# Performance work log

Hardware: AMD Instinct MI355X
Metric: run time of the kernel (lower is better)

Reference implementation:

```python
import jax, jax.numpy as jnp
import numpy as np

NUM_CLASSES = 21
OVERLAP_THRESH = 0.5
POS_PRIOR_THRESH = 0.01
NEGPOS_RATIO = 3
ARM_VAR = (0.1, 0.2)
VAR = (0.1, 0.2)
B, P, NOBJ = 64, 16320, 32


def _iou(a, b):
    # a: [N,4] point-form, b: [P,4] point-form -> [N,P]
    lt = jnp.maximum(a[:, None, :2], b[None, :, :2])
    rb = jnp.minimum(a[:, None, 2:], b[None, :, 2:])
    wh = jnp.clip(rb - lt, 0.0)
    inter = wh[..., 0] * wh[..., 1]
    area_a = (a[:, 2] - a[:, 0]) * (a[:, 3] - a[:, 1])
    area_b = (b[:, 2] - b[:, 0]) * (b[:, 3] - b[:, 1])
    return inter / (area_a[:, None] + area_b[None, :] - inter)


def _decode_point(loc, priors, var):
    # loc: [P,4], priors: [P,4] center-form -> [P,4] point-form
    cxcy = priors[:, :2] + loc[:, :2] * var[0] * priors[:, 2:]
    wh = priors[:, 2:] * jnp.exp(loc[:, 2:] * var[1])
    return jnp.concatenate([cxcy - wh / 2, cxcy + wh / 2], axis=-1)


def _encode(matched, priors, var):
    # matched: [P,4] point-form gt, priors: [P,4] center-form -> [P,4]
    g_cxcy = ((matched[:, :2] + matched[:, 2:]) / 2 - priors[:, :2]) / (var[0] * priors[:, 2:])
    g_wh = jnp.log((matched[:, 2:] - matched[:, :2]) / priors[:, 2:]) / var[1]
    return jnp.concatenate([g_cxcy, g_wh], axis=-1)


def _match_one(truths, labels, dec_point, ref_center, reserve):
    # truths:[N,4] labels:[N] dec_point/ref_center:[P,4] reserve:[P] bool
    n_obj = truths.shape[0]
    ov = _iou(truths, dec_point)                       # [N,P]
    ovm = jnp.where(reserve[None, :], ov, -1.0)        # mask out filtered priors
    best_prior_idx = jnp.argmax(ovm, axis=1)           # [N]
    best_truth_overlap = jnp.max(ovm, axis=0)          # [P]
    best_truth_idx = jnp.argmax(ovm, axis=0)           # [P]
    best_truth_overlap = best_truth_overlap.at[best_prior_idx].set(2.0)
    best_truth_idx = best_truth_idx.at[best_prior_idx].set(jnp.arange(n_obj))
    matched = truths[best_truth_idx]                   # [P,4]
    conf = labels[best_truth_idx] + 1                  # [P]
    conf = jnp.where(best_truth_overlap < OVERLAP_THRESH, 0, conf)
    loc = _encode(matched, ref_center, VAR)
    conf = jnp.where(reserve, conf, -1)                # ignored priors
    loc = jnp.where(reserve[:, None], loc, 0.0)
    return loc, conf


def setup_inputs() -> dict:
    key = jax.random.key(0)
    ks = jax.random.split(key, 8)
    arm_loc = 0.1 * jax.random.normal(ks[0], (B, P, 4), dtype=jnp.float32)
    arm_conf = jax.random.normal(ks[1], (B, P, 2), dtype=jnp.float32)
    odm_loc = jax.random.normal(ks[2], (B, P, 4), dtype=jnp.float32)
    odm_conf = jax.random.normal(ks[3], (B, P, NUM_CLASSES), dtype=jnp.float32)
    # center-form anchors: valid cx,cy,w,h
    cxcy = jax.random.uniform(ks[4], (P, 2), minval=0.02, maxval=0.98)
    wh = jax.random.uniform(ks[5], (P, 2), minval=0.05, maxval=0.4)
    priors = jnp.concatenate([cxcy, wh], axis=-1).astype(jnp.float32)
    # valid point-form ground-truth boxes
    tc = jax.random.uniform(ks[6], (B, NOBJ, 2), minval=0.2, maxval=0.8)
    tw = jax.random.uniform(ks[7], (B, NOBJ, 2), minval=0.05, maxval=0.3)
    truths = jnp.concatenate([tc - tw / 2, tc + tw / 2], axis=-1).astype(jnp.float32)
    labels = jax.random.randint(jax.random.fold_in(key, 9), (B, NOBJ), 0, 20)
    return {"arm_loc": arm_loc, "arm_conf": arm_conf, "odm_loc": odm_loc,
            "odm_conf": odm_conf, "priors": priors, "truths": truths,
            "labels": labels}


def reference(arm_loc, arm_conf, odm_loc, odm_conf, priors, truths, labels):
    # ARM branch and targets are constants w.r.t. gradients (torch uses .data)
    arm_loc = jax.lax.stop_gradient(arm_loc)
    arm_conf = jax.lax.stop_gradient(arm_conf)
    truths = jax.lax.stop_gradient(truths)
    priors = jax.lax.stop_gradient(priors)

    arm_pos_prob = jax.nn.softmax(arm_conf, axis=-1)[..., 1]       # [B,P]
    reserve = arm_pos_prob > POS_PRIOR_THRESH                      # [B,P]
    dec_point = jax.vmap(lambda l: _decode_point(l, priors, ARM_VAR))(arm_loc)  # [B,P,4]
    ref_center = jnp.concatenate([(dec_point[..., :2] + dec_point[..., 2:]) / 2,
                                  dec_point[..., 2:] - dec_point[..., :2]], axis=-1)
    loc_t, conf_t = jax.vmap(_match_one)(truths, labels, dec_point, ref_center, reserve)
    loc_t = jax.lax.stop_gradient(loc_t)
    conf_t = jax.lax.stop_gradient(conf_t)

    pos = conf_t > 0                                               # [B,P]
    ignore = conf_t == -1
    conf_t0 = jnp.where(ignore, 0, conf_t)

    # localization: smooth L1 over positives (sum)
    d = jnp.abs(odm_loc - loc_t)
    sl1 = jnp.where(d < 1.0, 0.5 * d * d, d - 0.5)
    loss_l = jnp.sum(sl1 * pos[..., None].astype(sl1.dtype))

    # per-prior CE: logsumexp - target logit
    lse = jax.nn.logsumexp(odm_conf, axis=-1)                      # [B,P]
    tgt = jnp.take_along_axis(odm_conf, conf_t0[..., None], axis=-1)[..., 0]
    ce = lse - tgt                                                 # [B,P]

    # hard-negative mining: rank negatives by CE (double argsort)
    mine = jnp.where(pos | ignore, 0.0, ce)
    order = jnp.argsort(-mine, axis=1)
    rank = jnp.argsort(order, axis=1)
    num_pos = jnp.sum(pos, axis=1, keepdims=True)                  # [B,1]
    num_neg = jnp.minimum(NEGPOS_RATIO * num_pos, P - 1)
    neg = rank < num_neg

    loss_c = jnp.sum(jnp.where(pos | neg, ce, 0.0))
    total_num = jnp.sum(num_pos).astype(jnp.float32)
    return (loss_l / total_num, loss_c / total_num)
```

## Files before the change

### kernel.cpp

```cpp
#include <hip/hip_runtime.h>

#define B 64
#define P 16320
#define NOBJ 32
#define NC 21

constexpr int T1 = 512;
constexpr int G1 = 4;
constexpr int C1 = T1 * G1;
constexpr int NP1 = (P + C1 - 1) / C1;
constexpr int BLK2 = 256;
constexpr int PBLK2 = (P + BLK2 - 1) / BLK2;
constexpr int TSEL = 1024;
__device__ constexpr float LN99 = 4.59511985013459f;

__global__ void k_init(unsigned long long* bp_packed, int* num_pos, float* ll_b, float* lc_b) {
    int t = threadIdx.x;
    for (int i = t; i < B * NOBJ; i += 256) bp_packed[i] = 0x407FFFFFFFFFFFFFULL;
    if (t < B) { num_pos[t] = 0; ll_b[t] = 0.f; lc_b[t] = 0.f; }
}

__global__ __launch_bounds__(T1) void k_phase1(
    const float* __restrict__ arm_loc, const float* __restrict__ arm_conf,
    const float* __restrict__ priors, const float* __restrict__ truths,
    int* __restrict__ bt_pack, unsigned long long* __restrict__ bp_packed)
{
    int b = blockIdx.y;
    int base = blockIdx.x * C1;
    int tid = threadIdx.x;
    __shared__ float4 tr4[NOBJ];
    __shared__ float tarea[NOBJ];
    __shared__ unsigned long long blk_best[NOBJ];
    if (tid < NOBJ) {
        float4 t = ((const float4*)truths)[b * NOBJ + tid];
        tr4[tid] = t;
        tarea[tid] = (t.z - t.x) * (t.w - t.y);
        blk_best[tid] = 0ULL;
    }
    __syncthreads();

    float x1[G1], y1[G1], x2[G1], y2[G1], areaP[G1];
    bool resv[G1], act[G1];
    float bestv[G1]; int bestj[G1];
    #pragma unroll
    for (int g = 0; g < G1; g++) {
        int p = base + g * T1 + tid;
        act[g] = p < P;
        resv[g] = false;
        x1[g] = y1[g] = x2[g] = y2[g] = 0.f; areaP[g] = 0.f;
        bestv[g] = -1.f; bestj[g] = 0;
        if (act[g]) {
            size_t bpi = (size_t)b * P + p;
            float2 cc = ((const float2*)arm_conf)[bpi];
            resv[g] = (cc.x - cc.y) < LN99;
            float4 l = ((const float4*)arm_loc)[bpi];
            float4 pr = ((const float4*)priors)[p];
            float dcx = pr.x + l.x * 0.1f * pr.z;
            float dcy = pr.y + l.y * 0.1f * pr.w;
            float dw = pr.z * __expf(l.z * 0.2f);
            float dh = pr.w * __expf(l.w * 0.2f);
            x1[g] = dcx - dw * 0.5f; y1[g] = dcy - dh * 0.5f;
            x2[g] = dcx + dw * 0.5f; y2[g] = dcy + dh * 0.5f;
            areaP[g] = (x2[g] - x1[g]) * (y2[g] - y1[g]);
        }
    }

    float val[NOBJ];
    unsigned gsel[2] = {0u, 0u};
    #pragma unroll
    for (int j = 0; j < NOBJ; j++) val[j] = -1.f;

    #pragma unroll
    for (int j = 0; j < NOBJ; j++) {
        float4 t = tr4[j];
        float ta = tarea[j];
        #pragma unroll
        for (int g = 0; g < G1; g++) {
            float iw = fmaxf(fminf(x2[g], t.z) - fmaxf(x1[g], t.x), 0.f);
            float ih = fmaxf(fminf(y2[g], t.w) - fmaxf(y1[g], t.y), 0.f);
            float inter = iw * ih;
            float iou = inter * __builtin_amdgcn_rcpf(ta + areaP[g] - inter);
            if (resv[g] && iou > bestv[g]) { bestv[g] = iou; bestj[g] = j; }
            if (resv[g] && iou > val[j]) {
                val[j] = iou;
                gsel[j >> 4] = (gsel[j >> 4] & ~(3u << (2 * (j & 15))))
                             | ((unsigned)g << (2 * (j & 15)));
            }
        }
    }

    #pragma unroll
    for (int g = 0; g < G1; g++) {
        if (act[g]) {
            int p = base + g * T1 + tid;
            int ge = (resv[g] && !(bestv[g] < 0.5f)) ? 1 : 0;
            bt_pack[(size_t)b * P + p] = (bestj[g] << 1) | ge;
        }
    }

    #pragma unroll
    for (int j = 0; j < NOBJ; j++) {
        unsigned g = (gsel[j >> 4] >> (2 * (j & 15))) & 3u;
        unsigned p = (unsigned)(base + (int)g * T1 + tid);
        unsigned long long pk = (val[j] >= 0.f)
            ? (((unsigned long long)(__float_as_uint(val[j]) | 0x80000000u) << 32)
               | (unsigned)~p)
            : 0ULL;
        #pragma unroll
        for (int off = 32; off; off >>= 1) {
            unsigned long long o = __shfl_xor(pk, off, 64);
            pk = o > pk ? o : pk;
        }
        if ((tid & 63) == 0 && pk) atomicMax(&blk_best[j], pk);
    }
    __syncthreads();
    if (tid < NOBJ && blk_best[tid]) atomicMax(&bp_packed[b * NOBJ + tid], blk_best[tid]);
}

__global__ __launch_bounds__(BLK2) void k_phase2(
    const float* __restrict__ arm_loc, const float* __restrict__ arm_conf,
    const float* __restrict__ odm_loc, const float* __restrict__ odm_conf,
    const float* __restrict__ priors, const float* __restrict__ truths,
    const int* __restrict__ labels, const int* __restrict__ bt_pack,
    const unsigned long long* __restrict__ bp_packed,
    float* __restrict__ mine, int* __restrict__ num_pos,
    float* __restrict__ ll_b, float* __restrict__ lc_b)
{
    int b = blockIdx.y;
    int p = blockIdx.x * BLK2 + threadIdx.x;
    __shared__ unsigned s_pi[NOBJ];
    __shared__ int s_lab[NOBJ];
    if (threadIdx.x < NOBJ) {
        s_pi[threadIdx.x] = ~(unsigned)(bp_packed[b * NOBJ + threadIdx.x] & 0xFFFFFFFFULL);
        s_lab[threadIdx.x] = labels[b * NOBJ + threadIdx.x];
    }
    __syncthreads();

    float ll = 0.f, lc = 0.f; int np = 0;
    if (p < P) {
        size_t bpi = (size_t)b * P + p;
        float2 cc = ((const float2*)arm_conf)[bpi];
        bool reserve = (cc.x - cc.y) < LN99;

        int pk = bt_pack[bpi];
        int bi = pk >> 1;
        int ge = pk & 1;
        #pragma unroll
        for (int j = 0; j < NOBJ; j++)
            if (s_pi[j] == (unsigned)p) { ge = 1; bi = j; }

        int conf = !reserve ? -1 : (ge ? s_lab[bi] + 1 : 0);

        const float* oc = odm_conf + bpi * NC;
        float vals[NC];
        #pragma unroll
        for (int k = 0; k < NC; k++) vals[k] = oc[k];
        float m = vals[0];
        #pragma unroll
        for (int k = 1; k < NC; k++) m = fmaxf(m, vals[k]);
        float s = 0.f;
        #pragma unroll
        for (int k = 0; k < NC; k++) s += __expf(vals[k] - m);
        int t0 = conf > 0 ? conf : 0;
        float ce = m + __logf(s) - oc[t0];

        bool pos = conf > 0;
        mine[bpi] = (pos || conf == -1) ? 0.f : ce;

        if (pos) {
            np = 1; lc = ce;
            float4 l = ((const float4*)arm_loc)[bpi];
            float4 pr = ((const float4*)priors)[p];
            float dcx = pr.x + l.x * 0.1f * pr.z;
            float dcy = pr.y + l.y * 0.1f * pr.w;
            float dw = pr.z * __expf(l.z * 0.2f);
            float dh = pr.w * __expf(l.w * 0.2f);
            float rx1 = dcx - dw * 0.5f, ry1 = dcy - dh * 0.5f;
            float rx2 = dcx + dw * 0.5f, ry2 = dcy + dh * 0.5f;
            float rcx = (rx1 + rx2) * 0.5f, rcy = (ry1 + ry2) * 0.5f;
            float rw = rx2 - rx1, rh = ry2 - ry1;
            float4 tb = ((const float4*)truths)[b * NOBJ + bi];
            float g0 = ((tb.x + tb.z) * 0.5f - rcx) * __builtin_amdgcn_rcpf(0.1f * rw);
            float g1 = ((tb.y + tb.w) * 0.5f - rcy) * __builtin_amdgcn_rcpf(0.1f * rh);
            float g2 = __logf((tb.z - tb.x) * __builtin_amdgcn_rcpf(rw)) * 5.0f;
            float g3 = __logf((tb.w - tb.y) * __builtin_amdgcn_rcpf(rh)) * 5.0f;
            float4 ol = ((const float4*)odm_loc)[bpi];
            float gt[4] = {g0, g1, g2, g3};
            float od[4] = {ol.x, ol.y, ol.z, ol.w};
            #pragma unroll
            for (int k = 0; k < 4; k++) {
                float d = fabsf(od[k] - gt[k]);
                ll += (d < 1.f) ? 0.5f * d * d : d - 0.5f;
            }
        }
    }

    #pragma unroll
    for (int off = 32; off; off >>= 1) {
        ll += __shfl_xor(ll, off, 64);
        lc += __shfl_xor(lc, off, 64);
        np += __shfl_xor(np, off, 64);
    }
    __shared__ float sll[BLK2 / 64], slc[BLK2 / 64];
    __shared__ int snp[BLK2 / 64];
    int wid = threadIdx.x >> 6, lane = threadIdx.x & 63;
    if (lane == 0) { sll[wid] = ll; slc[wid] = lc; snp[wid] = np; }
    __syncthreads();
    if (threadIdx.x == 0) {
        float a = 0.f, c = 0.f; int n = 0;
        for (int w = 0; w < BLK2 / 64; w++) { a += sll[w]; c += slc[w]; n += snp[w]; }
        if (a != 0.f) atomicAdd(&ll_b[b], a);
        if (c != 0.f) atomicAdd(&lc_b[b], c);
        if (n) atomicAdd(&num_pos[b], n);
    }
}

__global__ __launch_bounds__(TSEL) void k_select(
    const float* __restrict__ mine, const int* __restrict__ num_pos,
    float* __restrict__ lc_b)
{
    int b = blockIdx.x;
    int tid = threadIdx.x;
    int K0 = num_pos[b] * 3;
    if (K0 > P - 1) K0 = P - 1;
    if (K0 <= 0) return;
    const float* row = mine + (size_t)b * P;

    __shared__ unsigned hist[256];
    __shared__ unsigned sfx[256];
    __shared__ unsigned s_beta, s_K;

    unsigned K = (unsigned)K0;
    unsigned prefix = 0, maskDone = 0;

    for (int pass = 0; pass < 4; pass++) {
        int shift = 24 - pass * 8;
        if (tid < 256) hist[tid] = 0;
        __syncthreads();
        for (int i = tid; i < P; i += TSEL) {
            unsigned bits = __float_as_uint(row[i]);
            if ((bits & maskDone) == prefix) atomicAdd(&hist[(bits >> shift) & 255u], 1u);
        }
        __syncthreads();
        if (tid < 256) sfx[tid] = hist[tid];
        __syncthreads();
        for (int off = 1; off < 256; off <<= 1) {
            unsigned add = 0;
            if (tid < 256 && tid + off < 256) add = sfx[tid + off];
            __syncthreads();
            if (tid < 256) sfx[tid] += add;
            __syncthreads();
        }
        if (tid < 256) {
            unsigned Sc = sfx[tid];
            unsigned Sn = (tid < 255) ? sfx[tid + 1] : 0u;
            if (Sc >= K && Sn < K) { s_beta = (unsigned)tid; s_K = K - Sn; }
        }
        __syncthreads();
        prefix |= (s_beta << shift);
        maskDone |= (0xFFu << shift);
        K = s_K;
        __syncthreads();
    }

    unsigned tBits = prefix;
    float t = __uint_as_float(tBits);

    unsigned mcnt = 0; float ssum = 0.f;
    for (int i = tid; i < P; i += TSEL) {
        float v = row[i];
        if (__float_as_uint(v) > tBits) { mcnt++; ssum += v; }
    }
    #pragma unroll
    for (int off = 32; off; off >>= 1) {
        mcnt += __shfl_xor(mcnt, off, 64);
        ssum += __shfl_xor(ssum, off, 64);
    }
    __shared__ float sS[TSEL / 64];
    __shared__ unsigned sM[TSEL / 64];
    int wid = tid >> 6, lane = tid & 63;
    if (lane == 0) { sS[wid] = ssum; sM[wid] = mcnt; }
    __syncthreads();
    if (tid == 0) {
        float S = 0.f; unsigned M = 0;
        for (int w = 0; w < TSEL / 64; w++) { S += sS[w]; M += sM[w]; }
        float contrib = S + (float)(K0 - (int)M) * t;
        atomicAdd(&lc_b[b], contrib);
    }
}

__global__ void k_final(const int* __restrict__ num_pos, const float* __restrict__ ll_b,
                        const float* __restrict__ lc_b, float* __restrict__ out) {
    int t = threadIdx.x;
    int np = num_pos[t];
    float ll = ll_b[t];
    float lc = lc_b[t];
    #pragma unroll
    for (int off = 32; off; off >>= 1) {
        np += __shfl_xor(np, off, 64);
        ll += __shfl_xor(ll, off, 64);
        lc += __shfl_xor(lc, off, 64);
    }
    if (t == 0) {
        float tn = (float)np;
        out[0] = ll / tn;
        out[1] = lc / tn;
    }
}

extern "C" void kernel_launch(void* const* d_in, const int* in_sizes, int n_in,
                              void* d_out, int out_size, void* d_ws, size_t ws_size,
                              hipStream_t stream) {
    const float* arm_loc  = (const float*)d_in[0];
    const float* arm_conf = (const float*)d_in[1];
    const float* odm_loc  = (const float*)d_in[2];
    const float* odm_conf = (const float*)d_in[3];
    const float* priors   = (const float*)d_in[4];
    const float* truths   = (const float*)d_in[5];
    const int*   labels   = (const int*)d_in[6];
    float* out = (float*)d_out;

    char* ws = (char*)d_ws;
    const size_t BPTOT = (size_t)B * P;
    int*   bt_pack = (int*)ws;
    float* mine    = (float*)(ws + 4ull * BPTOT);
    unsigned long long* bp_packed = (unsigned long long*)(ws + 8ull * BPTOT);
    int*   num_pos = (int*)(ws + 8ull * BPTOT + 8ull * B * NOBJ);
    float* ll_b    = (float*)(ws + 8ull * BPTOT + 8ull * B * NOBJ + 4ull * B);
    float* lc_b    = (float*)(ws + 8ull * BPTOT + 8ull * B * NOBJ + 8ull * B);

    k_init<<<1, 256, 0, stream>>>(bp_packed, num_pos, ll_b, lc_b);
    k_phase1<<<dim3(NP1, B), T1, 0, stream>>>(arm_loc, arm_conf, priors, truths,
                                              bt_pack, bp_packed);
    k_phase2<<<dim3(PBLK2, B), BLK2, 0, stream>>>(arm_loc, arm_conf, odm_loc, odm_conf,
                                                  priors, truths, labels, bt_pack,
                                                  bp_packed, mine, num_pos, ll_b, lc_b);
    k_select<<<B, TSEL, 0, stream>>>(mine, num_pos, lc_b);
    k_final<<<1, 64, 0, stream>>>(num_pos, ll_b, lc_b, out);
}
```

Baseline: 262.3 us.

## Restructure matching: per-truth-group best-prior kernel, recompute IoU in phase2, stage logits in LDS

Phase 1 now only computes the best prior per truth. Each block handles one image and one group of 8 truths, looping over all priors and reducing in shared memory without global atomics. Phase 2 recomputes the per-prior best-truth IoU itself, which drops the bt_pack intermediate write and read, and stages the odm_conf logits in shared memory for coalesced loads. The top-k selection kernel moves to 256 threads with a wave-shuffle suffix scan. The trade is redundant IoU work in phase 2 and a phase 1 grid of only 256 blocks that loop serially over P.

```diff
diff --git a/kernel.cpp b/kernel.cpp
--- a/kernel.cpp
+++ b/kernel.cpp
@@ -5,181 +5,198 @@
 #define NOBJ 32
 #define NC 21
 
-constexpr int T1 = 512;
-constexpr int G1 = 4;
-constexpr int C1 = T1 * G1;
-constexpr int NP1 = (P + C1 - 1) / C1;
-constexpr int BLK2 = 256;
-constexpr int PBLK2 = (P + BLK2 - 1) / BLK2;
-constexpr int TSEL = 1024;
 __device__ constexpr float LN99 = 4.59511985013459f;
 
-__global__ void k_init(unsigned long long* bp_packed, int* num_pos, float* ll_b, float* lc_b) {
+__global__ void k_init(int* num_pos, float* ll_b, float* lc_b) {
     int t = threadIdx.x;
-    for (int i = t; i < B * NOBJ; i += 256) bp_packed[i] = 0x407FFFFFFFFFFFFFULL;
     if (t < B) { num_pos[t] = 0; ll_b[t] = 0.f; lc_b[t] = 0.f; }
 }
 
-__global__ __launch_bounds__(T1) void k_phase1(
+__global__ __launch_bounds__(1024) void k_p1b(
     const float* __restrict__ arm_loc, const float* __restrict__ arm_conf,
     const float* __restrict__ priors, const float* __restrict__ truths,
-    int* __restrict__ bt_pack, unsigned long long* __restrict__ bp_packed)
+    unsigned long long* __restrict__ bp_packed)
+{
+    int jg = blockIdx.x >> 6;
+    int b  = blockIdx.x & 63;
+    int tid = threadIdx.x;
+    __shared__ unsigned long long s1[8 * 512];
+    __shared__ unsigned long long s2[64];
+
+    float4 T[8]; float TA[8];
+    #pragma unroll
+    for (int jj = 0; jj < 8; jj++) {
+        T[jj] = ((const float4*)truths)[b * NOBJ + jg * 8 + jj];
+        TA[jj] = (T[jj].z - T[jj].x) * (T[jj].w - T[jj].y);
+    }
+    unsigned long long key[8];
+    #pragma unroll
+    for (int jj = 0; jj < 8; jj++) key[jj] = 0x407FFFFFFFFFFFFFULL;
+
+    for (int i = tid; i < P; i += 1024) {
+        size_t bpi = (size_t)b * P + i;
+        float2 cc = ((const float2*)arm_conf)[bpi];
+        bool resv = (cc.x - cc.y) < LN99;
+        float4 l = ((const float4*)arm_loc)[bpi];
+        float4 pr = ((const float4*)priors)[i];
+        float dcx = pr.x + l.x * 0.1f * pr.z;
+        float dcy = pr.y + l.y * 0.1f * pr.w;
+        float dw = pr.z * __expf(l.z * 0.2f);
+        float dh = pr.w * __expf(l.w * 0.2f);
+        float x1 = dcx - dw * 0.5f;
+        float y1 = dcy - dh * 0.5f;
+        float x2 = dcx + dw * 0.5f;
+        float y2 = dcy + dh * 0.5f;
+        float areaP = (x2 - x1) * (y2 - y1);
+        #pragma unroll
+        for (int jj = 0; jj < 8; jj++) {
+            float iw = fmaxf(fminf(x2, T[jj].z) - fmaxf(x1, T[jj].x), 0.f);
+            float ih = fmaxf(fminf(y2, T[jj].w) - fmaxf(y1, T[jj].y), 0.f);
+            float inter = iw * ih;
+            float iou = inter * __builtin_amdgcn_rcpf(TA[jj] + areaP - inter);
+            unsigned long long k =
+                ((unsigned long long)(__float_as_uint(iou) | 0x80000000u) << 32)
+                | (unsigned)~(unsigned)i;
+            if (resv && k > key[jj]) key[jj] = k;
+        }
+    }
+
+    #pragma unroll
+    for (int jj = 0; jj < 8; jj++) {
+        unsigned long long o = __shfl_xor(key[jj], 1, 64);
+        if (o > key[jj]) key[jj] = o;
+    }
+    if ((tid & 1) == 0) {
+        #pragma unroll
+        for (int jj = 0; jj < 8; jj++) s1[jj * 512 + (tid >> 1)] = key[jj];
+    }
+    __syncthreads();
+
+    unsigned long long m1 = 0;
+    {
+        int j = tid >> 7, c = tid & 127;
+        #pragma unroll
+        for (int i = 0; i < 4; i++) {
+            unsigned long long v = s1[j * 512 + c * 4 + ((i + c) & 3)];
+            if (v > m1) m1 = v;
+        }
+    }
+    __syncthreads();
+    s1[tid] = m1;
+    __syncthreads();
+
+    if (tid < 64) {
+        int j = tid >> 3, c = tid & 7;
+        unsigned long long m2 = 0;
+        #pragma unroll
+        for (int i = 0; i < 16; i++) {
+            unsigned long long v = s1[j * 128 + c * 16 + ((i + c) & 15)];
+            if (v > m2) m2 = v;
+        }
+        s2[tid] = m2;
+    }
+    __syncthreads();
+
+    if (tid < 8) {
+        unsigned long long m3 = 0;
+        #pragma unroll
+        for (int i = 0; i < 8; i++) {
+            unsigned long long v = s2[tid * 8 + ((i + tid) & 7)];
+            if (v > m3) m3 = v;
+        }
+        bp_packed[b * NOBJ + jg * 8 + tid] = m3;
+    }
+}
+
+__global__ __launch_bounds__(256) void k_p2(
+    const float* __restrict__ arm_loc, const float* __restrict__ arm_conf,
+    const float* __restrict__ odm_loc, const float* __restrict__ odm_conf,
+    const float* __restrict__ priors, const float* __restrict__ truths,
+    const int* __restrict__ labels,
+    const unsigned long long* __restrict__ bp_packed,
+    float* __restrict__ mine, int* __restrict__ num_pos,
+    float* __restrict__ ll_b, float* __restrict__ lc_b)
 {
     int b = blockIdx.y;
-    int base = blockIdx.x * C1;
+    int pbase = blockIdx.x * 256;
     int tid = threadIdx.x;
-    __shared__ float4 tr4[NOBJ];
-    __shared__ float tarea[NOBJ];
-    __shared__ unsigned long long blk_best[NOBJ];
+    int p = pbase + tid;
+
+    __shared__ float soc[256 * NC];
+    __shared__ float4 s_tr[NOBJ];
+    __shared__ float s_ta[NOBJ];
+    __shared__ unsigned s_pi[NOBJ];
+    __shared__ int s_lab[NOBJ];
+
     if (tid < NOBJ) {
         float4 t = ((const float4*)truths)[b * NOBJ + tid];
-        tr4[tid] = t;
-        tarea[tid] = (t.z - t.x) * (t.w - t.y);
-        blk_best[tid] = 0ULL;
-    }
-    __syncthreads();
-
-    float x1[G1], y1[G1], x2[G1], y2[G1], areaP[G1];
-    bool resv[G1], act[G1];
-    float bestv[G1]; int bestj[G1];
-    #pragma unroll
-    for (int g = 0; g < G1; g++) {
-        int p = base + g * T1 + tid;
-        act[g] = p < P;
-        resv[g] = false;
-        x1[g] = y1[g] = x2[g] = y2[g] = 0.f; areaP[g] = 0.f;
-        bestv[g] = -1.f; bestj[g] = 0;
-        if (act[g]) {
-            size_t bpi = (size_t)b * P + p;
-            float2 cc = ((const float2*)arm_conf)[bpi];
-            resv[g] = (cc.x - cc.y) < LN99;
+        s_tr[tid] = t;
+        s_ta[tid] = (t.z - t.x) * (t.w - t.y);
+        s_pi[tid] = ~(unsigned)(bp_packed[b * NOBJ + tid] & 0xFFFFFFFFULL);
+        s_lab[tid] = labels[b * NOBJ + tid];
+    }
+    {
+        int nval = P - pbase; if (nval > 256) nval = 256;
+        int tot = nval * NC;
+        const float* ocb = odm_conf + ((size_t)b * P + pbase) * NC;
+        for (int i = tid; i < tot; i += 256) soc[i] = ocb[i];
+    }
+    __syncthreads();
+
+    float ll = 0.f, lc = 0.f; int np = 0;
+    if (p < P) {
+        size_t bpi = (size_t)b * P + p;
+        float2 cc = ((const float2*)arm_conf)[bpi];
+        bool resv = (cc.x - cc.y) < LN99;
+
+        int bi = 0; bool ge = false;
+        float rx1 = 0.f, ry1 = 0.f, rx2 = 0.f, ry2 = 0.f;
+        if (resv) {
             float4 l = ((const float4*)arm_loc)[bpi];
             float4 pr = ((const float4*)priors)[p];
             float dcx = pr.x + l.x * 0.1f * pr.z;
             float dcy = pr.y + l.y * 0.1f * pr.w;
             float dw = pr.z * __expf(l.z * 0.2f);
             float dh = pr.w * __expf(l.w * 0.2f);
-            x1[g] = dcx - dw * 0.5f; y1[g] = dcy - dh * 0.5f;
-            x2[g] = dcx + dw * 0.5f; y2[g] = dcy + dh * 0.5f;
-            areaP[g] = (x2[g] - x1[g]) * (y2[g] - y1[g]);
-        }
-    }
-
-    float val[NOBJ];
-    unsigned gsel[2] = {0u, 0u};
-    #pragma unroll
-    for (int j = 0; j < NOBJ; j++) val[j] = -1.f;
-
-    #pragma unroll
-    for (int j = 0; j < NOBJ; j++) {
-        float4 t = tr4[j];
-        float ta = tarea[j];
-        #pragma unroll
-        for (int g = 0; g < G1; g++) {
-            float iw = fmaxf(fminf(x2[g], t.z) - fmaxf(x1[g], t.x), 0.f);
-            float ih = fmaxf(fminf(y2[g], t.w) - fmaxf(y1[g], t.y), 0.f);
-            float inter = iw * ih;
-            float iou = inter * __builtin_amdgcn_rcpf(ta + areaP[g] - inter);
-            if (resv[g] && iou > bestv[g]) { bestv[g] = iou; bestj[g] = j; }
-            if (resv[g] && iou > val[j]) {
-                val[j] = iou;
-                gsel[j >> 4] = (gsel[j >> 4] & ~(3u << (2 * (j & 15))))
-                             | ((unsigned)g << (2 * (j & 15)));
+            rx1 = dcx - dw * 0.5f; ry1 = dcy - dh * 0.5f;
+            rx2 = dcx + dw * 0.5f; ry2 = dcy + dh * 0.5f;
+            float areaP = (rx2 - rx1) * (ry2 - ry1);
+            float bestv = -1.f;
+            #pragma unroll
+            for (int j = 0; j < NOBJ; j++) {
+                float4 t = s_tr[j];
+                float iw = fmaxf(fminf(rx2, t.z) - fmaxf(rx1, t.x), 0.f);
+                float ih = fmaxf(fminf(ry2, t.w) - fmaxf(ry1, t.y), 0.f);
+                float inter = iw * ih;
+                float iou = inter * __builtin_amdgcn_rcpf(s_ta[j] + areaP - inter);
+                if (iou > bestv) { bestv = iou; bi = j; }
             }
-        }
-    }
-
-    #pragma unroll
-    for (int g = 0; g < G1; g++) {
-        if (act[g]) {
-            int p = base + g * T1 + tid;
-            int ge = (resv[g] && !(bestv[g] < 0.5f)) ? 1 : 0;
-            bt_pack[(size_t)b * P + p] = (bestj[g] << 1) | ge;
-        }
-    }
-
-    #pragma unroll
-    for (int j = 0; j < NOBJ; j++) {
-        unsigned g = (gsel[j >> 4] >> (2 * (j & 15))) & 3u;
-        unsigned p = (unsigned)(base + (int)g * T1 + tid);
-        unsigned long long pk = (val[j] >= 0.f)
-            ? (((unsigned long long)(__float_as_uint(val[j]) | 0x80000000u) << 32)
-               | (unsigned)~p)
-            : 0ULL;
-        #pragma unroll
-        for (int off = 32; off; off >>= 1) {
-            unsigned long long o = __shfl_xor(pk, off, 64);
-            pk = o > pk ? o : pk;
-        }
-        if ((tid & 63) == 0 && pk) atomicMax(&blk_best[j], pk);
-    }
-    __syncthreads();
-    if (tid < NOBJ && blk_best[tid]) atomicMax(&bp_packed[b * NOBJ + tid], blk_best[tid]);
-}
-
-__global__ __launch_bounds__(BLK2) void k_phase2(
-    const float* __restrict__ arm_loc, const float* __restrict__ arm_conf,
-    const float* __restrict__ odm_loc, const float* __restrict__ odm_conf,
-    const float* __restrict__ priors, const float* __restrict__ truths,
-    const int* __restrict__ labels, const int* __restrict__ bt_pack,
-    const unsigned long long* __restrict__ bp_packed,
-    float* __restrict__ mine, int* __restrict__ num_pos,
-    float* __restrict__ ll_b, float* __restrict__ lc_b)
-{
-    int b = blockIdx.y;
-    int p = blockIdx.x * BLK2 + threadIdx.x;
-    __shared__ unsigned s_pi[NOBJ];
-    __shared__ int s_lab[NOBJ];
-    if (threadIdx.x < NOBJ) {
-        s_pi[threadIdx.x] = ~(unsigned)(bp_packed[b * NOBJ + threadIdx.x] & 0xFFFFFFFFULL);
-        s_lab[threadIdx.x] = labels[b * NOBJ + threadIdx.x];
-    }
-    __syncthreads();
-
-    float ll = 0.f, lc = 0.f; int np = 0;
-    if (p < P) {
-        size_t bpi = (size_t)b * P + p;
-        float2 cc = ((const float2*)arm_conf)[bpi];
-        bool reserve = (cc.x - cc.y) < LN99;
-
-        int pk = bt_pack[bpi];
-        int bi = pk >> 1;
-        int ge = pk & 1;
+            ge = !(bestv < 0.5f);
+        }
         #pragma unroll
         for (int j = 0; j < NOBJ; j++)
-            if (s_pi[j] == (unsigned)p) { ge = 1; bi = j; }
-
-        int conf = !reserve ? -1 : (ge ? s_lab[bi] + 1 : 0);
-
-        const float* oc = odm_conf + bpi * NC;
-        float vals[NC];
-        #pragma unroll
-        for (int k = 0; k < NC; k++) vals[k] = oc[k];
-        float m = vals[0];
-        #pragma unroll
-        for (int k = 1; k < NC; k++) m = fmaxf(m, vals[k]);
+            if (s_pi[j] == (unsigned)p) { ge = true; bi = j; }
+
+        int conf = !resv ? -1 : (ge ? s_lab[bi] + 1 : 0);
+
+        const float* row = &soc[tid * NC];
+        float m = row[0];
+        #pragma unroll
+        for (int k = 1; k < NC; k++) m = fmaxf(m, row[k]);
         float s = 0.f;
         #pragma unroll
-        for (int k = 0; k < NC; k++) s += __expf(vals[k] - m);
+        for (int k = 0; k < NC; k++) s += __expf(row[k] - m);
         int t0 = conf > 0 ? conf : 0;
-        float ce = m + __logf(s) - oc[t0];
+        float ce = m + __logf(s) - row[t0];
 
         bool pos = conf > 0;
         mine[bpi] = (pos || conf == -1) ? 0.f : ce;
 
         if (pos) {
             np = 1; lc = ce;
-            float4 l = ((const float4*)arm_loc)[bpi];
-            float4 pr = ((const float4*)priors)[p];
-            float dcx = pr.x + l.x * 0.1f * pr.z;
-            float dcy = pr.y + l.y * 0.1f * pr.w;
-            float dw = pr.z * __expf(l.z * 0.2f);
-            float dh = pr.w * __expf(l.w * 0.2f);
-            float rx1 = dcx - dw * 0.5f, ry1 = dcy - dh * 0.5f;
-            float rx2 = dcx + dw * 0.5f, ry2 = dcy + dh * 0.5f;
             float rcx = (rx1 + rx2) * 0.5f, rcy = (ry1 + ry2) * 0.5f;
             float rw = rx2 - rx1, rh = ry2 - ry1;
-            float4 tb = ((const float4*)truths)[b * NOBJ + bi];
+            float4 tb = s_tr[bi];
             float g0 = ((tb.x + tb.z) * 0.5f - rcx) * __builtin_amdgcn_rcpf(0.1f * rw);
             float g1 = ((tb.y + tb.w) * 0.5f - rcy) * __builtin_amdgcn_rcpf(0.1f * rh);
             float g2 = __logf((tb.z - tb.x) * __builtin_amdgcn_rcpf(rw)) * 5.0f;
@@ -201,21 +218,21 @@
         lc += __shfl_xor(lc, off, 64);
         np += __shfl_xor(np, off, 64);
     }
-    __shared__ float sll[BLK2 / 64], slc[BLK2 / 64];
-    __shared__ int snp[BLK2 / 64];
-    int wid = threadIdx.x >> 6, lane = threadIdx.x & 63;
+    __shared__ float sll[4], slc[4];
+    __shared__ int snp[4];
+    int wid = tid >> 6, lane = tid & 63;
     if (lane == 0) { sll[wid] = ll; slc[wid] = lc; snp[wid] = np; }
     __syncthreads();
-    if (threadIdx.x == 0) {
+    if (tid == 0) {
         float a = 0.f, c = 0.f; int n = 0;
-        for (int w = 0; w < BLK2 / 64; w++) { a += sll[w]; c += slc[w]; n += snp[w]; }
+        for (int w = 0; w < 4; w++) { a += sll[w]; c += slc[w]; n += snp[w]; }
         if (a != 0.f) atomicAdd(&ll_b[b], a);
         if (c != 0.f) atomicAdd(&lc_b[b], c);
         if (n) atomicAdd(&num_pos[b], n);
     }
 }
 
-__global__ __launch_bounds__(TSEL) void k_select(
+__global__ __launch_bounds__(256) void k_select(
     const float* __restrict__ mine, const int* __restrict__ num_pos,
     float* __restrict__ lc_b)
 {
@@ -227,7 +244,6 @@
     const float* row = mine + (size_t)b * P;
 
     __shared__ unsigned hist[256];
-    __shared__ unsigned sfx[256];
     __shared__ unsigned s_beta, s_K;
 
     unsigned K = (unsigned)K0;
@@ -235,26 +251,29 @@
 
     for (int pass = 0; pass < 4; pass++) {
         int shift = 24 - pass * 8;
-        if (tid < 256) hist[tid] = 0;
+        hist[tid] = 0;
         __syncthreads();
-        for (int i = tid; i < P; i += TSEL) {
+        for (int i = tid; i < P; i += 256) {
             unsigned bits = __float_as_uint(row[i]);
             if ((bits & maskDone) == prefix) atomicAdd(&hist[(bits >> shift) & 255u], 1u);
         }
         __syncthreads();
-        if (tid < 256) sfx[tid] = hist[tid];
-        __syncthreads();
-        for (int off = 1; off < 256; off <<= 1) {
-            unsigned add = 0;
-            if (tid < 256 && tid + off < 256) add = sfx[tid + off];
-            __syncthreads();
-            if (tid < 256) sfx[tid] += add;
-            __syncthreads();
-        }
-        if (tid < 256) {
-            unsigned Sc = sfx[tid];
-            unsigned Sn = (tid < 255) ? sfx[tid + 1] : 0u;
-            if (Sc >= K && Sn < K) { s_beta = (unsigned)tid; s_K = K - Sn; }
+        if (tid < 64) {
+            unsigned u0 = hist[tid * 4 + 0], u1 = hist[tid * 4 + 1];
+            unsigned u2 = hist[tid * 4 + 2], u3 = hist[tid * 4 + 3];
+            unsigned sum4 = u0 + u1 + u2 + u3;
+            unsigned x = sum4;
+            #pragma unroll
+            for (int off = 1; off < 64; off <<= 1) {
+                unsigned y = __shfl_down(x, off, 64);
+                if (tid + off < 64) x += y;
+            }
+            unsigned sf0 = x, sf1 = x - u0, sf2 = x - u0 - u1, sf3 = x - u0 - u1 - u2;
+            unsigned sf4 = x - sum4;
+            if (sf0 >= K && sf1 < K) { s_beta = tid * 4 + 0; s_K = K - sf1; }
+            if (sf1 >= K && sf2 < K) { s_beta = tid * 4 + 1; s_K = K - sf2; }
+            if (sf2 >= K && sf3 < K) { s_beta = tid * 4 + 2; s_K = K - sf3; }
+            if (sf3 >= K && sf4 < K) { s_beta = tid * 4 + 3; s_K = K - sf4; }
         }
         __syncthreads();
         prefix |= (s_beta << shift);
@@ -267,7 +286,7 @@
     float t = __uint_as_float(tBits);
 
     unsigned mcnt = 0; float ssum = 0.f;
-    for (int i = tid; i < P; i += TSEL) {
+    for (int i = tid; i < P; i += 256) {
         float v = row[i];
         if (__float_as_uint(v) > tBits) { mcnt++; ssum += v; }
     }
@@ -276,16 +295,15 @@
         mcnt += __shfl_xor(mcnt, off, 64);
         ssum += __shfl_xor(ssum, off, 64);
     }
-    __shared__ float sS[TSEL / 64];
-    __shared__ unsigned sM[TSEL / 64];
+    __shared__ float sS[4];
+    __shared__ unsigned sM[4];
     int wid = tid >> 6, lane = tid & 63;
     if (lane == 0) { sS[wid] = ssum; sM[wid] = mcnt; }
     __syncthreads();
     if (tid == 0) {
         float S = 0.f; unsigned M = 0;
-        for (int w = 0; w < TSEL / 64; w++) { S += sS[w]; M += sM[w]; }
-        float contrib = S + (float)(K0 - (int)M) * t;
-        atomicAdd(&lc_b[b], contrib);
+        for (int w = 0; w < 4; w++) { S += sS[w]; M += sM[w]; }
+        atomicAdd(&lc_b[b], S + (float)(K0 - (int)M) * t);
     }
 }
 
@@ -322,19 +340,17 @@
 
     char* ws = (char*)d_ws;
     const size_t BPTOT = (size_t)B * P;
-    int*   bt_pack = (int*)ws;
-    float* mine    = (float*)(ws + 4ull * BPTOT);
-    unsigned long long* bp_packed = (unsigned long long*)(ws + 8ull * BPTOT);
-    int*   num_pos = (int*)(ws + 8ull * BPTOT + 8ull * B * NOBJ);
-    float* ll_b    = (float*)(ws + 8ull * BPTOT + 8ull * B * NOBJ + 4ull * B);
-    float* lc_b    = (float*)(ws + 8ull * BPTOT + 8ull * B * NOBJ + 8ull * B);
-
-    k_init<<<1, 256, 0, stream>>>(bp_packed, num_pos, ll_b, lc_b);
-    k_phase1<<<dim3(NP1, B), T1, 0, stream>>>(arm_loc, arm_conf, priors, truths,
-                                              bt_pack, bp_packed);
-    k_phase2<<<dim3(PBLK2, B), BLK2, 0, stream>>>(arm_loc, arm_conf, odm_loc, odm_conf,
-                                                  priors, truths, labels, bt_pack,
-                                                  bp_packed, mine, num_pos, ll_b, lc_b);
-    k_select<<<B, TSEL, 0, stream>>>(mine, num_pos, lc_b);
+    float* mine = (float*)ws;
+    unsigned long long* bp_packed = (unsigned long long*)(ws + 4ull * BPTOT);
+    int*   num_pos = (int*)(ws + 4ull * BPTOT + 8ull * B * NOBJ);
+    float* ll_b    = (float*)(ws + 4ull * BPTOT + 8ull * B * NOBJ + 4ull * B);
+    float* lc_b    = (float*)(ws + 4ull * BPTOT + 8ull * B * NOBJ + 8ull * B);
+
+    k_init<<<1, 64, 0, stream>>>(num_pos, ll_b, lc_b);
+    k_p1b<<<256, 1024, 0, stream>>>(arm_loc, arm_conf, priors, truths, bp_packed);
+    k_p2<<<dim3(64, B), 256, 0, stream>>>(arm_loc, arm_conf, odm_loc, odm_conf,
+                                          priors, truths, labels, bp_packed,
+                                          mine, num_pos, ll_b, lc_b);
+    k_select<<<B, 256, 0, stream>>>(mine, num_pos, lc_b);
     k_final<<<1, 64, 0, stream>>>(num_pos, ll_b, lc_b, out);
 }
```

Result: slower. 281.9 us (+7.5%).
